# Optimization experiments

Hardware: AMD Instinct MI355X
Metric: run time of the kernel (lower is better)

## Reference

```python
import jax, jax.numpy as jnp
import numpy as np
from math import factorial

IRREPS = [0] * 256 + [1] * 256 + [2] * 128 + [3] * 64
N_BATCH, CHANNELS = 1024, 32


def _dfact(n):
    r = 1
    while n > 1:
        r *= n
        n -= 2
    return r


def _sh_l(l, xyz):
    """Real spherical harmonics of degree l, components m=-l..l, at unit vectors xyz."""
    x, y, z = xyz[:, 0], xyz[:, 1], xyz[:, 2]
    phi = np.arctan2(y, x)
    ct = z
    st = np.sqrt(np.clip(1.0 - ct * ct, 0.0, None))
    Y = np.zeros((xyz.shape[0], 2 * l + 1))
    for m in range(l + 1):
        pmm = ((-1.0) ** m) * _dfact(2 * m - 1) * st ** m  # P_m^m(cos t)
        if l == m:
            plm = pmm
        else:
            pm1 = ct * (2 * m + 1) * pmm  # P_{m+1}^m
            if l == m + 1:
                plm = pm1
            else:
                p2, p1 = pmm, pm1
                for ll in range(m + 2, l + 1):
                    p2, p1 = p1, ((2 * ll - 1) * ct * p1 - (ll + m - 1) * p2) / (ll - m)
                plm = p1
        K = np.sqrt((2 * l + 1) / (4 * np.pi) * factorial(l - m) / factorial(l + m))
        if m == 0:
            Y[:, l] = K * plm
        else:
            Y[:, l + m] = np.sqrt(2.0) * K * np.cos(m * phi) * plm
            Y[:, l - m] = np.sqrt(2.0) * K * np.sin(m * phi) * plm
    return Y


def _j_matrix(l):
    """Orthogonal involution J_l: real-SH matrix of the y<->z axis swap (J = J^T = J^-1)."""
    rng = np.random.default_rng(0)
    v = rng.normal(size=(max(256, 16 * (2 * l + 1)), 3))
    v /= np.linalg.norm(v, axis=1, keepdims=True)
    A = _sh_l(l, v)
    B = _sh_l(l, v[:, [0, 2, 1]])  # Y(swap r)
    X, _, _, _ = np.linalg.lstsq(A, B, rcond=None)
    return X.T  # Y(swap r) = J @ Y(r)


def _build_info():
    freq, rev, groups = [], [], []
    off = 0
    i = 0
    while i < len(IRREPS):
        l = IRREPS[i]
        mul = 0
        while i < len(IRREPS) and IRREPS[i] == l:
            mul += 1
            i += 1
        d = 2 * l + 1
        groups.append((l, off, mul, np.asarray(_j_matrix(l), np.float32)))
        for _ in range(mul):
            for k in range(d):
                freq.append(k - l)      # m value of component k
                rev.append(off + (d - 1 - k))  # index of the -m partner
            off += d
    return np.asarray(freq, np.float32), np.asarray(rev, np.int32), groups, off


FREQ_NP, REV_NP, GROUPS, DIM = _build_info()
FREQ = jnp.asarray(FREQ_NP)
REV = jnp.asarray(REV_NP)
J_MATS = [jnp.asarray(J) for (_, _, _, J) in GROUPS]


def _z_rot(x, theta):
    """Per-m z-rotation (sparse vecsca): out_m = cos(m t) x_m - sin(m t) x_{-m}."""
    ang = theta[:, None] * FREQ  # (N, DIM)
    return jnp.cos(ang)[..., None] * x - jnp.sin(ang)[..., None] * x[:, REV, :]


def _j_apply(x):
    """Block-diagonal J application, grouped by l (sparse scale / flip stage)."""
    n, _, c = x.shape
    outs = []
    for (l, off, mul, _), J in zip(GROUPS, J_MATS):
        d = 2 * l + 1
        seg = x[:, off:off + mul * d, :].reshape(n, mul, d, c)
        outs.append(jnp.einsum('pq,nmqc->nmpc', J, seg).reshape(n, mul * d, c))
    return jnp.concatenate(outs, axis=1)


def setup_inputs() -> dict:
    key = jax.random.key(0)
    k0, k1, k2, k3 = jax.random.split(key, 4)
    two_pi = 2.0 * np.pi
    return {
        'input': jax.random.normal(k0, (N_BATCH, DIM, CHANNELS), dtype=jnp.float32),
        'alpha': jax.random.uniform(k1, (N_BATCH,), dtype=jnp.float32) * two_pi,
        'beta': jax.random.uniform(k2, (N_BATCH,), dtype=jnp.float32) * two_pi,
        'gamma': jax.random.uniform(k3, (N_BATCH,), dtype=jnp.float32) * two_pi,
    }


def reference(input, alpha, beta, gamma):
    # D(alpha, beta, gamma) = Dz(alpha) J Dz(beta) J Dz(gamma)
    x = _z_rot(input, gamma)
    x = _j_apply(x)
    x = _z_rot(x, beta)
    x = _j_apply(x)
    return _z_rot(x, alpha)
```

## Files before the change

### kernel.cpp

```cpp
#include <hip/hip_runtime.h>
#include <math.h>


namespace {

typedef float f4 __attribute__((ext_vector_type(4)));

constexpr float SQ3_2 = 0.86602540378443864676f;
constexpr float S6    = 0.61237243569579452455f;
constexpr float S10   = 0.79056941504209483300f;
constexpr float S15   = 0.96824583655185422129f;

template<int L> struct JM;
template<> struct JM<1> {
  static constexpr float v[3][3] = {
    { 0.f, -1.f, 0.f},
    {-1.f,  0.f, 0.f},
    { 0.f,  0.f, 1.f}};
};
template<> struct JM<2> {
  static constexpr float v[5][5] = {
    { 0.f, 0.f,  0.f,   -1.f,  0.f},
    { 0.f, 1.f,  0.f,    0.f,  0.f},
    { 0.f, 0.f, -0.5f,   0.f, -SQ3_2},
    {-1.f, 0.f,  0.f,    0.f,  0.f},
    { 0.f, 0.f, -SQ3_2,  0.f,  0.5f}};
};
template<> struct JM<3> {
  static constexpr float v[7][7] = {
    { 0.f, 0.f, 0.f, S10,  0.f,   -S6,  0.f},
    { 0.f, 1.f, 0.f, 0.f,  0.f,    0.f, 0.f},
    { 0.f, 0.f, 0.f, S6,   0.f,    S10, 0.f},
    { S10, 0.f, S6,  0.f,  0.f,    0.f, 0.f},
    { 0.f, 0.f, 0.f, 0.f, -0.25f,  0.f, -S15},
    {-S6,  0.f, S10, 0.f,  0.f,    0.f, 0.f},
    { 0.f, 0.f, 0.f, 0.f, -S15,    0.f, 0.25f}};
};

template<int L>
__device__ inline void compute_M_col(int q, float al, float be, float ga, float* M) {
  constexpr int D = 2 * L + 1;
  const int mq = q - L;
  float sg, cg;
  sincosf((float)mq * ga, &sg, &cg);
  float v[D];
#pragma unroll
  for (int p = 0; p < D; ++p)
    v[p] = cg * JM<L>::v[p][q] + sg * JM<L>::v[p][(D - 1) - q];
  float c1, s1;
  sincosf(be, &s1, &c1);
  float cb[L + 1], sb[L + 1];
  cb[0] = 1.f; sb[0] = 0.f;
  cb[1] = c1;  sb[1] = s1;
#pragma unroll
  for (int k = 2; k <= L; ++k) {
    cb[k] = 2.f * c1 * cb[k - 1] - cb[k - 2];
    sb[k] = 2.f * c1 * sb[k - 1] - sb[k - 2];
  }
  float w[D];
#pragma unroll
  for (int p = 0; p < D; ++p) {
    const int mp = p - L;
    const int am = mp < 0 ? -mp : mp;
    const float c = cb[am];
    const float s = mp < 0 ? -sb[am] : sb[am];
    w[p] = c * v[p] - s * v[(D - 1) - p];
  }
  float u[D];
#pragma unroll
  for (int p = 0; p < D; ++p) {
    float acc = 0.f;
#pragma unroll
    for (int r = 0; r < D; ++r) acc = fmaf(JM<L>::v[p][r], w[r], acc);
    u[p] = acc;
  }
  sincosf(al, &s1, &c1);
  float ca[L + 1], sa[L + 1];
  ca[0] = 1.f; sa[0] = 0.f;
  ca[1] = c1;  sa[1] = s1;
#pragma unroll
  for (int k = 2; k <= L; ++k) {
    ca[k] = 2.f * c1 * ca[k - 1] - ca[k - 2];
    sa[k] = 2.f * c1 * sa[k - 1] - sa[k - 2];
  }
#pragma unroll
  for (int p = 0; p < D; ++p) {
    const int mp = p - L;
    const int am = mp < 0 ? -mp : mp;
    const float c = ca[am];
    const float s = mp < 0 ? -sa[am] : sa[am];
    M[p * D + q] = c * u[p] - s * u[(D - 1) - p];
  }
}

__global__ __launch_bounds__(256) void build_M_kernel(
    const float* __restrict__ alpha, const float* __restrict__ beta,
    const float* __restrict__ gamma, float* __restrict__ ws, int n_batch) {
  const int t = threadIdx.x;
  const int n = blockIdx.x * 16 + (t >> 4);
  const int col = t & 15;
  if (n >= n_batch || col >= 15) return;
  const float al = alpha[n], be = beta[n], ga = gamma[n];
  float* w = ws + (size_t)n * 96;
  if (col < 7)       compute_M_col<3>(col,      al, be, ga, w);
  else if (col < 12) compute_M_col<2>(col - 7,  al, be, ga, w + 49);
  else               compute_M_col<1>(col - 12, al, be, ga, w + 74);
}

template<int D>
__device__ inline void apply_block(const f4* __restrict__ inN,
                                   f4* __restrict__ outN,
                                   const float* __restrict__ M, int off, int ch) {
  f4 v[D];
#pragma unroll
  for (int q = 0; q < D; ++q)
    v[q] = __builtin_nontemporal_load(&inN[(off + q) * 8 + ch]);
#pragma unroll
  for (int p = 0; p < D; ++p) {
    f4 a = M[p * D] * v[0];
#pragma unroll
    for (int q = 1; q < D; ++q) a += M[p * D + q] * v[q];
    __builtin_nontemporal_store(a, &outN[(off + p) * 8 + ch]);
  }
}

__device__ inline void stream_body(const float* __restrict__ in,
                                   float* __restrict__ out,
                                   const float* __restrict__ M,
                                   int n, int t) {
  const float* M3 = M;
  const float* M2 = M + 49;
  const float* M1 = M + 74;
  const size_t base = (size_t)n * (2112 * 8);
  const f4* inN = (const f4*)in + base;
  f4* outN = (f4*)out + base;
  const int g = t >> 3;
  const int ch = t & 7;

#pragma unroll
  for (int j = 0; j < 4; ++j) {
    const int r = 64 * j + g;
    __builtin_nontemporal_store(__builtin_nontemporal_load(&inN[r * 8 + ch]),
                                &outN[r * 8 + ch]);
  }
#pragma unroll
  for (int j = 0; j < 4; ++j)
    apply_block<3>(inN, outN, M1, 256 + 3 * (64 * j + g), ch);
#pragma unroll
  for (int j = 0; j < 2; ++j)
    apply_block<5>(inN, outN, M2, 1024 + 5 * (64 * j + g), ch);
  apply_block<7>(inN, outN, M3, 1664 + 7 * g, ch);
}

__global__ __launch_bounds__(512, 8) void wigner_stream_kernel(
    const float* __restrict__ in, const float* __restrict__ ws,
    float* __restrict__ out) {
  __shared__ float M[96];
  const int n = blockIdx.x;
  const int t = threadIdx.x;
  if (t < 83) M[t] = ws[(size_t)n * 96 + t];
  __syncthreads();
  stream_body(in, out, M, n, t);
}

__global__ __launch_bounds__(512) void wigner_fused_kernel(
    const float* __restrict__ in, const float* __restrict__ alpha,
    const float* __restrict__ beta, const float* __restrict__ gamma,
    float* __restrict__ out) {
  __shared__ float M[96];
  const int n = blockIdx.x;
  const int t = threadIdx.x;
  if (t < 15) {
    const float al = alpha[n], be = beta[n], ga = gamma[n];
    if (t < 7)       compute_M_col<3>(t,      al, be, ga, M);
    else if (t < 12) compute_M_col<2>(t - 7,  al, be, ga, M + 49);
    else             compute_M_col<1>(t - 12, al, be, ga, M + 74);
  }
  __syncthreads();
  stream_body(in, out, M, n, t);
}

}

extern "C" void kernel_launch(void* const* d_in, const int* in_sizes, int n_in,
                              void* d_out, int out_size, void* d_ws, size_t ws_size,
                              hipStream_t stream) {
  const float* in    = (const float*)d_in[0];
  const float* alpha = (const float*)d_in[1];
  const float* beta  = (const float*)d_in[2];
  const float* gamma = (const float*)d_in[3];
  float* out = (float*)d_out;
  const int n_batch = in_sizes[1];

  const size_t ws_needed = (size_t)n_batch * 96 * sizeof(float);
  if (ws_size >= ws_needed) {
    float* ws = (float*)d_ws;
    build_M_kernel<<<(n_batch + 15) / 16, 256, 0, stream>>>(alpha, beta, gamma,
                                                            ws, n_batch);
    wigner_stream_kernel<<<n_batch, 512, 0, stream>>>(in, ws, out);
  } else {
    wigner_fused_kernel<<<n_batch, 512, 0, stream>>>(in, alpha, beta, gamma, out);
  }
}
```

Measured before the change: 117.0 us.

## Stage irrep blocks through LDS with async global-to-LDS loads in chunks

Replaces the per-thread register gather of D rows per block with chunked staging: each section (l=1,2,3) is copied into a shared buffer using global_load_lds 16-byte async loads, then each thread computes one output float4 by reading its block's D rows from LDS. Output and input accesses become fully contiguous per chunk, and nontemporal hints are dropped. It adds two block-wide barriers per chunk, 28 KB of LDS per block (occupancy hint lowered to 4), and removes the fused fallback path when the workspace is too small.

New measurement: 120.9 us. 1.03x slower.

```diff
diff --git a/kernel.cpp b/kernel.cpp
--- a/kernel.cpp
+++ b/kernel.cpp
@@ -107,77 +107,65 @@
   else               compute_M_col<1>(col - 12, al, be, ga, w + 74);
 }
 
-template<int D>
-__device__ inline void apply_block(const f4* __restrict__ inN,
-                                   f4* __restrict__ outN,
-                                   const float* __restrict__ M, int off, int ch) {
-  f4 v[D];
+__device__ inline void gload16(const void* g, void* l) {
+  __builtin_amdgcn_global_load_lds(
+      (const __attribute__((address_space(1))) void*)g,
+      (__attribute__((address_space(3))) void*)l, 16, 0, 0);
+}
+
+template<int D, int CHUNK_ROWS, int NCHUNK>
+__device__ inline void apply_section(const f4* __restrict__ inSec,
+                                     f4* __restrict__ outSec,
+                                     const float* __restrict__ M,
+                                     f4* __restrict__ buf, int t) {
+  constexpr int F = CHUNK_ROWS * 8;
+  constexpr int ITER = (F + 511) / 512;
+  for (int c = 0; c < NCHUNK; ++c) {
+    const f4* src = inSec + c * F;
 #pragma unroll
-  for (int q = 0; q < D; ++q)
-    v[q] = __builtin_nontemporal_load(&inN[(off + q) * 8 + ch]);
+    for (int i = 0; i < ITER; ++i) {
+      const int k = t + 512 * i;
+      if (k < F) gload16(src + k, buf + k);
+    }
+    __syncthreads();
+    f4* dst = outSec + c * F;
 #pragma unroll
-  for (int p = 0; p < D; ++p) {
-    f4 a = M[p * D] * v[0];
+    for (int i = 0; i < ITER; ++i) {
+      const int k = t + 512 * i;
+      if (k < F) {
+        const int r = k >> 3;
+        const int p = r % D;
+        const float* Mrow = M + p * D;
+        const f4* b = buf + (k - p * 8);
+        f4 a = Mrow[0] * b[0];
 #pragma unroll
-    for (int q = 1; q < D; ++q) a += M[p * D + q] * v[q];
-    __builtin_nontemporal_store(a, &outN[(off + p) * 8 + ch]);
+        for (int q = 1; q < D; ++q) a += Mrow[q] * b[q * 8];
+        dst[k] = a;
+      }
+    }
+    __syncthreads();
   }
 }
 
-__device__ inline void stream_body(const float* __restrict__ in,
-                                   float* __restrict__ out,
-                                   const float* __restrict__ M,
-                                   int n, int t) {
-  const float* M3 = M;
-  const float* M2 = M + 49;
-  const float* M1 = M + 74;
-  const size_t base = (size_t)n * (2112 * 8);
-  const f4* inN = (const f4*)in + base;
-  f4* outN = (f4*)out + base;
-  const int g = t >> 3;
-  const int ch = t & 7;
-
-#pragma unroll
-  for (int j = 0; j < 4; ++j) {
-    const int r = 64 * j + g;
-    __builtin_nontemporal_store(__builtin_nontemporal_load(&inN[r * 8 + ch]),
-                                &outN[r * 8 + ch]);
-  }
-#pragma unroll
-  for (int j = 0; j < 4; ++j)
-    apply_block<3>(inN, outN, M1, 256 + 3 * (64 * j + g), ch);
-#pragma unroll
-  for (int j = 0; j < 2; ++j)
-    apply_block<5>(inN, outN, M2, 1024 + 5 * (64 * j + g), ch);
-  apply_block<7>(inN, outN, M3, 1664 + 7 * g, ch);
-}
-
-__global__ __launch_bounds__(512, 8) void wigner_stream_kernel(
+__global__ __launch_bounds__(512, 4) void wigner_stream_kernel(
     const float* __restrict__ in, const float* __restrict__ ws,
     float* __restrict__ out) {
+  __shared__ f4 buf[1792];
   __shared__ float M[96];
   const int n = blockIdx.x;
   const int t = threadIdx.x;
   if (t < 83) M[t] = ws[(size_t)n * 96 + t];
-  __syncthreads();
-  stream_body(in, out, M, n, t);
-}
 
-__global__ __launch_bounds__(512) void wigner_fused_kernel(
-    const float* __restrict__ in, const float* __restrict__ alpha,
-    const float* __restrict__ beta, const float* __restrict__ gamma,
-    float* __restrict__ out) {
-  __shared__ float M[96];
-  const int n = blockIdx.x;
-  const int t = threadIdx.x;
-  if (t < 15) {
-    const float al = alpha[n], be = beta[n], ga = gamma[n];
-    if (t < 7)       compute_M_col<3>(t,      al, be, ga, M);
-    else if (t < 12) compute_M_col<2>(t - 7,  al, be, ga, M + 49);
-    else             compute_M_col<1>(t - 12, al, be, ga, M + 74);
-  }
-  __syncthreads();
-  stream_body(in, out, M, n, t);
+  const size_t base = (size_t)n * (2112 * 8);
+  const f4* inN = (const f4*)in + base;
+  f4* outN = (f4*)out + base;
+
+#pragma unroll
+  for (int i = 0; i < 4; ++i) outN[t + 512 * i] = inN[t + 512 * i];
+
+  apply_section<3, 192, 4>(inN + 256 * 8, outN + 256 * 8, M + 74, buf, t);
+  apply_section<5, 160, 4>(inN + 1024 * 8, outN + 1024 * 8, M + 49, buf, t);
+  apply_section<7, 224, 2>(inN + 1664 * 8, outN + 1664 * 8, M, buf, t);
 }
 
 }
@@ -192,13 +180,8 @@
   float* out = (float*)d_out;
   const int n_batch = in_sizes[1];
 
-  const size_t ws_needed = (size_t)n_batch * 96 * sizeof(float);
-  if (ws_size >= ws_needed) {
-    float* ws = (float*)d_ws;
-    build_M_kernel<<<(n_batch + 15) / 16, 256, 0, stream>>>(alpha, beta, gamma,
-                                                            ws, n_batch);
-    wigner_stream_kernel<<<n_batch, 512, 0, stream>>>(in, ws, out);
-  } else {
-    wigner_fused_kernel<<<n_batch, 512, 0, stream>>>(in, alpha, beta, gamma, out);
-  }
+  float* ws = (float*)d_ws;
+  build_M_kernel<<<(n_batch + 15) / 16, 256, 0, stream>>>(alpha, beta, gamma,
+                                                          ws, n_batch);
+  wigner_stream_kernel<<<n_batch, 512, 0, stream>>>(in, ws, out);
 }
```
